# Kernel tuning notes

Measured on AMD Instinct MI355X. Metric: run time of the kernel, lower is better.

The kernel has to match this reference:

```python
import jax, jax.numpy as jnp
import numpy as np

B, L, D = 1, 2048, 1024
H, E = 16, 64        # n_heads, d_head
ROT = E // 2         # rotary half-dim
FF = 4 * D
EPS = 1e-6
NEG = -1e30


def setup_inputs() -> dict:
    key = jax.random.key(0)
    ks = jax.random.split(key, 6)
    x = jax.random.normal(ks[0], (B, L, D), jnp.float32)
    theta = jax.random.uniform(ks[1], (B, H, L, ROT), jnp.float32) * (2.0 * np.pi)
    scale = jax.random.normal(ks[2], (B, D), jnp.float32) * 0.1
    w_in = jax.random.normal(ks[3], (7 * D, D), jnp.float32) * (D ** -0.5)
    w_out = jax.random.normal(ks[4], (D, 5 * D), jnp.float32) * ((5 * D) ** -0.5)
    attn_scale = jnp.full((2, H), 10.0, jnp.float32)
    return {"x": x, "theta": theta, "scale": scale,
            "w_in": w_in, "w_out": w_out, "attn_scale": attn_scale}


def _rope(t, cos, sin):
    # t: [b,h,l,E]; rotary applied to first 2*ROT dims (== E here, so no passthrough)
    t1, t2 = t[..., :ROT], t[..., ROT:2 * ROT]
    return jnp.concatenate([t1 * cos - t2 * sin, t2 * cos + t1 * sin], axis=-1)


def _forward(x, theta, scale, w_in, w_out, attn_scale):
    b, l, d = x.shape
    skip = x
    # AdaRMSNorm (no learned weight): rms-normalize then modulate by (1 + scale)
    xn = x * jax.lax.rsqrt(jnp.mean(x ** 2, axis=-1, keepdims=True) + EPS)
    xn = xn * (1.0 + scale[:, None, :])
    # fused QKV + MLP-up projection (torch Linear: y = x @ W.T)
    proj = jnp.einsum('bld,fd->blf', xn, w_in)       # [b,l,7d]
    qkv, up = proj[..., :3 * d], proj[..., 3 * d:]
    up = jax.nn.gelu(up, approximate=True)           # GELU(tanh)
    # 'b l (t nh e) -> t b nh l e'
    qkv = qkv.reshape(b, l, 3, H, E).transpose(2, 0, 3, 1, 4)
    q, k, v = qkv[0], qkv[1], qkv[2]
    # cosine-sim rescaling: q_h * sqrt(s_h)/||q||, k_h * sqrt(s_h)/||k||
    s = jnp.sqrt(attn_scale[0])[None, :, None, None]
    q = q * (s * jax.lax.rsqrt(jnp.sum(q ** 2, axis=-1, keepdims=True) + EPS))
    k = k * (s * jax.lax.rsqrt(jnp.sum(k ** 2, axis=-1, keepdims=True) + EPS))
    # rotary embedding
    cos, sin = jnp.cos(theta), jnp.sin(theta)
    q, k = _rope(q, cos, sin), _rope(k, cos, sin)
    # causal attention with scale = 1.0 (cosine-sim path)
    scores = jnp.einsum('bhqe,bhke->bhqk', q, k)
    causal = jnp.tril(jnp.ones((l, l), bool))
    scores = jnp.where(causal[None, None], scores, NEG)
    probs = jax.nn.softmax(scores, axis=-1)
    attn = jnp.einsum('bhqk,bhke->bhqe', probs, v)
    attn_out = attn.transpose(0, 2, 1, 3).reshape(b, l, d)  # 'b nh l e -> b l (nh e)'
    h = jnp.concatenate([attn_out, up], axis=-1)            # [b,l,5d]
    return jnp.einsum('blf,df->bld', h, w_out) + skip


def reference(x, theta, scale, w_in, w_out, attn_scale):
    return _forward(x, theta, scale, w_in, w_out, attn_scale)
```

## Files before the change

### kernel.cpp

```cpp
#include <hip/hip_runtime.h>

typedef unsigned short u16;
typedef unsigned int u32;
typedef __attribute__((ext_vector_type(8))) short bf16x8;
typedef __attribute__((ext_vector_type(8))) unsigned short u16x8;
typedef __attribute__((ext_vector_type(4))) float f32x4;
typedef __attribute__((ext_vector_type(16))) float f32x16;

#define L_SEQ 2048
#define DMODEL 1024
#define NHEAD 16
#define EHEAD 64
#define FPROJ 7168
#define FCAT 5120
#define NEGINF -1e30f
#define LOG2E 1.44269504088896f
#define EXP2F(x) __builtin_amdgcn_exp2f(x)

__device__ __forceinline__ u16 f2bf(float f) {
  union { float f; u32 u; } v; v.f = f;
  u32 r = v.u + 0x7FFFu + ((v.u >> 16) & 1u);
  return (u16)(r >> 16);
}
__device__ __forceinline__ float bf2f(u16 h) {
  union { u32 u; float f; } v; v.u = ((u32)h) << 16;
  return v.f;
}
__device__ __forceinline__ float gelu_f(float x) {
  float y = 0.7978845608028654f * (x + 0.044715f * x * x * x);
  float t = __expf(-2.0f * fabsf(y));
  float th = (1.0f - t) / (1.0f + t);
  th = (y < 0.0f) ? -th : th;
  return 0.5f * x * (1.0f + th);
}
__device__ __forceinline__ void gld16(void* lds, const void* g) {
  __builtin_amdgcn_global_load_lds((const __attribute__((address_space(1))) u32*)g,
                                   (__attribute__((address_space(3))) u32*)lds, 16, 0, 0);
}

__global__ __launch_bounds__(256) void cvt2_kernel(const float* __restrict__ a,
                                                   u16* __restrict__ oa, int na4,
                                                   const float* __restrict__ b,
                                                   u16* __restrict__ ob, int nb4) {
  int i = blockIdx.x * 256 + threadIdx.x;
  const float* src;
  u16* dst;
  int j;
  if (i < na4) {
    src = a; dst = oa; j = i;
  } else {
    j = i - na4;
    if (j >= nb4) return;
    src = b; dst = ob;
  }
  float4 v = ((const float4*)src)[j];
  ((u32*)dst)[2 * j] = (u32)f2bf(v.x) | ((u32)f2bf(v.y) << 16);
  ((u32*)dst)[2 * j + 1] = (u32)f2bf(v.z) | ((u32)f2bf(v.w) << 16);
}

__global__ __launch_bounds__(256) void rmsnorm_kernel(const float* __restrict__ x,
                                                      const float* __restrict__ scale,
                                                      u16* __restrict__ xn) {
  int row = blockIdx.x;
  const float4 v = ((const float4*)(x + (size_t)row * DMODEL))[threadIdx.x];
  float ss = v.x * v.x + v.y * v.y + v.z * v.z + v.w * v.w;
#pragma unroll
  for (int m = 1; m < 64; m <<= 1) ss += __shfl_xor(ss, m);
  __shared__ float ws[4];
  if ((threadIdx.x & 63) == 0) ws[threadIdx.x >> 6] = ss;
  __syncthreads();
  float tot = ws[0] + ws[1] + ws[2] + ws[3];
  float r = rsqrtf(tot * (1.0f / DMODEL) + 1e-6f);
  float4 sc = ((const float4*)scale)[threadIdx.x];
  u32 w0 = (u32)f2bf(v.x * r * (1.0f + sc.x)) | ((u32)f2bf(v.y * r * (1.0f + sc.y)) << 16);
  u32 w1 = (u32)f2bf(v.z * r * (1.0f + sc.z)) | ((u32)f2bf(v.w * r * (1.0f + sc.w)) << 16);
  u32* dst = (u32*)(xn + (size_t)row * DMODEL);
  dst[2 * threadIdx.x] = w0;
  dst[2 * threadIdx.x + 1] = w1;
}

__device__ __forceinline__ void stage_half(u16* lds, const u16* g, int K, int tid) {
#pragma unroll
  for (int i = 0; i < 2; ++i) {
    int idx = tid + i * 512;
    int r = idx >> 3;
    int gcb = ((idx & 7) << 4) ^ ((r & 7) << 4);
    gld16((char*)lds + idx * 16, (const char*)g + (size_t)r * K * 2 + gcb);
  }
}

#define GFENCE asm volatile("" ::: "memory")
#define VMW0 asm volatile("s_waitcnt vmcnt(0)" ::: "memory")
#define ST_A(BUF, T, HALF) stage_half(sA + (BUF) * 16384 + (HALF) * 8192, \
    Ab + (size_t)((HALF) * 128) * K + (T) * 64, K, tid)
#define ST_B(BUF, T, HALF) stage_half(sB + (BUF) * 16384 + (HALF) * 8192, \
    Bb + (size_t)((HALF) * 128) * K + (T) * 64, K, tid)

#define PHASE(KH, BUFB, WCODE, STCODE) do { \
    const char* ab_ = (const char*)sA + (BUFB) * 32768 + wm * 16384 + frow * 128 + ((KH) ? co1 : co0); \
    const char* bb_ = (const char*)sB + (BUFB) * 32768 + (wn2 >> 1) * 16384 + ((wn2 & 1) * 64 + frow) * 128 + ((KH) ? co1 : co0); \
    bf16x8 af_[8], bv_[4]; \
    _Pragma("unroll") \
    for (int mr = 0; mr < 8; ++mr) af_[mr] = *(const bf16x8*)(ab_ + mr * 2048); \
    _Pragma("unroll") \
    for (int nr = 0; nr < 4; ++nr) bv_[nr] = *(const bf16x8*)(bb_ + nr * 2048); \
    GFENCE; \
    STCODE; \
    WCODE; \
    __builtin_amdgcn_s_barrier(); \
    __builtin_amdgcn_s_setprio(1); \
    _Pragma("unroll") \
    for (int mr = 0; mr < 8; ++mr) \
      _Pragma("unroll") \
      for (int nr = 0; nr < 4; ++nr) \
        acc[mr][nr] = __builtin_amdgcn_mfma_f32_16x16x32_bf16(af_[mr], bv_[nr], acc[mr][nr], 0, 0, 0); \
    __builtin_amdgcn_s_setprio(0); \
    __builtin_amdgcn_s_barrier(); \
  } while (0)

template <int OUTMODE>
__global__ __launch_bounds__(512, 2) void gemm256(const u16* __restrict__ A,
                                                  const u16* __restrict__ B,
                                                  u16* __restrict__ C0,
                                                  u16* __restrict__ C1,
                                                  int M, int N, int K) {
  __shared__ __align__(16) u16 sA[2 * 16384];
  __shared__ __align__(16) u16 sB[2 * 16384];
  const int tid = threadIdx.x;
  const int lane = tid & 63;
  const int wv = tid >> 6;
  const int wm = wv >> 2;
  const int wn2 = wv & 3;
  const int frow = lane & 15;
  const int kbyte = ((lane >> 4) & 3) << 4;
  const int sw = (frow & 7) << 4;
  const int co0 = kbyte ^ sw;
  const int co1 = (64 | kbyte) ^ sw;

  const int nbx = N >> 8;
  const int nbm = (int)gridDim.x / nbx;
  const int v = (blockIdx.x & 7) * ((int)gridDim.x >> 3) + ((int)blockIdx.x >> 3);
  const int bm = v % nbm, bn = v / nbm;
  const int kper = K / (int)gridDim.y;
  const int kbeg = blockIdx.y * kper;
  const u16* Ab = A + (size_t)(bm * 256) * K + kbeg;
  const u16* Bb = B + (size_t)(bn * 256) * K + kbeg;

  f32x4 acc[8][4] = {};

  const int NT = kper >> 6;
  ST_A(0, 0, 0); ST_A(0, 0, 1); ST_B(0, 0, 0); ST_B(0, 0, 1);
  VMW0;
  __builtin_amdgcn_s_barrier();

  for (int kt = 0; kt < NT; kt += 2) {
    const int t1 = kt + 1;
    const int t2 = (kt + 2 >= NT) ? 0 : kt + 2;
    PHASE(0, 0, , ST_A(1, t1, 0); ST_A(1, t1, 1); ST_B(1, t1, 0); ST_B(1, t1, 1));
    PHASE(1, 0, VMW0, );
    PHASE(0, 1, , ST_A(0, t2, 0); ST_A(0, t2, 1); ST_B(0, t2, 0); ST_B(0, t2, 1));
    PHASE(1, 1, VMW0, );
  }

  if (OUTMODE == 1) {
    const bool up = (bn >= 12);
#pragma unroll
    for (int mr = 0; mr < 8; ++mr) {
#pragma unroll
      for (int nr = 0; nr < 4; ++nr) {
        int grow = bm * 256 + wm * 128 + mr * 16 + ((lane >> 4) * 4);
        int gcol = bn * 256 + wn2 * 64 + nr * 16 + frow;
        if (!up) {
          u16* cp = C0 + (size_t)grow * (3 * DMODEL) + gcol;
#pragma unroll
          for (int r = 0; r < 4; ++r) cp[(size_t)r * (3 * DMODEL)] = f2bf(acc[mr][nr][r]);
        } else {
          u16* cp = C1 + (size_t)grow * FCAT + (gcol - 2048);
#pragma unroll
          for (int r = 0; r < 4; ++r) cp[(size_t)r * FCAT] = f2bf(gelu_f(acc[mr][nr][r]));
        }
      }
    }
  } else {
    u16* Cp = C0 + (size_t)blockIdx.y * M * N;
#pragma unroll
    for (int mr = 0; mr < 8; ++mr) {
#pragma unroll
      for (int nr = 0; nr < 4; ++nr) {
        int grow = bm * 256 + wm * 128 + mr * 16 + ((lane >> 4) * 4);
        int gcol = bn * 256 + wn2 * 64 + nr * 16 + frow;
        u16* cp = Cp + (size_t)grow * N + gcol;
#pragma unroll
        for (int r = 0; r < 4; ++r) cp[(size_t)r * N] = f2bf(acc[mr][nr][r]);
      }
    }
  }
}

__global__ __launch_bounds__(256) void combine8(const u16* __restrict__ part,
                                                const float* __restrict__ x,
                                                float* __restrict__ out) {
  size_t i = (size_t)(blockIdx.x * 256 + threadIdx.x) * 8;
  float4 x0 = *(const float4*)(x + i);
  float4 x1 = *(const float4*)(x + i + 4);
  float s[8] = {x0.x, x0.y, x0.z, x0.w, x1.x, x1.y, x1.z, x1.w};
#pragma unroll
  for (int p = 0; p < 8; ++p) {
    u16x8 v = *(const u16x8*)(part + (size_t)p * (L_SEQ * DMODEL) + i);
#pragma unroll
    for (int j = 0; j < 8; ++j) s[j] += bf2f(v[j]);
  }
  float4 o0 = {s[0], s[1], s[2], s[3]};
  float4 o1 = {s[4], s[5], s[6], s[7]};
  *(float4*)(out + i) = o0;
  *(float4*)(out + i + 4) = o1;
}

__global__ __launch_bounds__(256) void qkv_prep(const u16* __restrict__ proj,
                                                const float* __restrict__ theta,
                                                const float* __restrict__ attn_scale,
                                                u16* __restrict__ qb, u16* __restrict__ kb,
                                                u16* __restrict__ vb) {
  const int l = blockIdx.x * 4 + (threadIdx.x >> 6);
  const int hd = blockIdx.y;
  const int e = threadIdx.x & 63;
  const u16* pr = proj + (size_t)l * (3 * DMODEL) + hd * EHEAD + e;
  float q = bf2f(pr[0]);
  float k = bf2f(pr[DMODEL]);
  float v = bf2f(pr[2 * DMODEL]);
  float sq = q * q, sk = k * k;
#pragma unroll
  for (int m = 1; m < 64; m <<= 1) {
    sq += __shfl_xor(sq, m);
    sk += __shfl_xor(sk, m);
  }
  float s = sqrtf(attn_scale[hd]);
  q *= LOG2E * s * rsqrtf(sq + 1e-6f);
  k *= s * rsqrtf(sk + 1e-6f);
  float ang = theta[((size_t)hd * L_SEQ + l) * 32 + (e & 31)];
  float cs = __cosf(ang), sn = __sinf(ang);
  float qp = __shfl_xor(q, 32), kp = __shfl_xor(k, 32);
  float qr = (e < 32) ? (q * cs - qp * sn) : (q * cs + qp * sn);
  float kr = (e < 32) ? (k * cs - kp * sn) : (k * cs + kp * sn);
  size_t o = ((size_t)hd * L_SEQ + l) * EHEAD + e;
  qb[o] = f2bf(qr);
  kb[o] = f2bf(kr);
  vb[o] = f2bf(v);
}

__global__ __launch_bounds__(128, 4) void attn_kernel(const u16* __restrict__ qb,
                                                      const u16* __restrict__ kb,
                                                      const u16* __restrict__ vb,
                                                      u16* __restrict__ po,
                                                      float* __restrict__ pm,
                                                      float* __restrict__ pl) {
  const int bid = blockIdx.x;
  const int s = 31 - (bid >> 6);
  const int hd = (bid >> 2) & 15;
  const int c = bid & 3;
  const int tid = threadIdx.x;
  const int lane = tid & 63;
  const int w = tid >> 6;
  const int h = lane >> 5;
  const int ql = lane & 31;
  const int qg = s * 64 + w * 32 + ql;
  const int nt = s + 1;
  const int t0 = (c * nt) >> 2;
  const int t1 = ((c + 1) * nt) >> 2;

  __shared__ u16 sK[64 * 64];
  __shared__ u16 sVT[64 * 64];

  const u16* Kh = kb + (size_t)hd * L_SEQ * EHEAD;
  const u16* Vh = vb + (size_t)hd * L_SEQ * EHEAD;
  const u16* Qh = qb + (size_t)hd * L_SEQ * EHEAD;

  bf16x8 qf[4];
#pragma unroll
  for (int es = 0; es < 4; ++es)
    qf[es] = *(const bf16x8*)(Qh + (size_t)qg * EHEAD + es * 16 + h * 8);

  f32x16 oa[2] = {};
  float m = NEGINF, lsum = 0.0f;

  const int vk = (tid & 15) * 4;
  const int ve = (tid >> 4) * 8;

  for (int kt = t0; kt < t1; ++kt) {
    const int k0 = kt * 64;
    __syncthreads();
#pragma unroll
    for (int i = 0; i < 4; ++i) {
      int r = w * 32 + i * 8 + (lane >> 3);
      const u16* src = Kh + (size_t)(k0 + r) * EHEAD + (((lane & 7) ^ (r & 7)) << 3);
      gld16(sK + (w * 32 + i * 8) * 64 + lane * 8, src);
    }
    u16x8 vr[4];
#pragma unroll
    for (int j = 0; j < 4; ++j)
      vr[j] = *(const u16x8*)(Vh + (size_t)(k0 + vk + j) * EHEAD + ve);
#pragma unroll
    for (int e = 0; e < 8; ++e) {
      int row = ve + e;
      int boff = row * 128 + ((((vk >> 3) ^ (row & 7)) << 4) | ((vk & 4) << 1));
      ushort4 pv;
      pv.x = vr[0][e]; pv.y = vr[1][e]; pv.z = vr[2][e]; pv.w = vr[3][e];
      *(ushort4*)((char*)sVT + boff) = pv;
    }
    __syncthreads();

    f32x16 st[2];
#pragma unroll
    for (int t = 0; t < 2; ++t) {
      f32x16 a = {};
      __builtin_amdgcn_s_setprio(1);
#pragma unroll
      for (int es = 0; es < 4; ++es) {
        int row = t * 32 + ql;
        int boff = row * 128 + (((es * 2 + h) ^ (row & 7)) << 4);
        bf16x8 kf = *(const bf16x8*)((const char*)sK + boff);
        a = __builtin_amdgcn_mfma_f32_32x32x16_bf16(kf, qf[es], a, 0, 0, 0);
      }
      __builtin_amdgcn_s_setprio(0);
      st[t] = a;
    }

    float p[2][16];
    float mx = NEGINF;
    const bool edge = (kt == s);
#pragma unroll
    for (int t = 0; t < 2; ++t)
#pragma unroll
      for (int r = 0; r < 16; ++r) {
        float v = st[t][r];
        if (edge) {
          int kg = k0 + t * 32 + (r & 3) + ((r >> 2) << 3) + h * 4;
          v = (kg > qg) ? NEGINF : v;
        }
        p[t][r] = v;
        mx = fmaxf(mx, v);
      }
    mx = fmaxf(mx, __shfl_xor(mx, 32));
    if (!__all(mx - m <= 8.0f)) {
      float mnew = fmaxf(m, mx);
      float alpha = EXP2F(m - mnew);
      lsum *= alpha;
#pragma unroll
      for (int et = 0; et < 2; ++et)
#pragma unroll
        for (int r = 0; r < 16; ++r) oa[et][r] *= alpha;
      m = mnew;
    }
    float ps = 0.0f;
#pragma unroll
    for (int t = 0; t < 2; ++t)
#pragma unroll
      for (int r = 0; r < 16; ++r) {
        float e_ = EXP2F(p[t][r] - m);
        p[t][r] = e_;
        ps += e_;
      }
    ps += __shfl_xor(ps, 32);
    lsum += ps;

    u32 pk_[2][8];
#pragma unroll
    for (int t = 0; t < 2; ++t)
#pragma unroll
      for (int i = 0; i < 8; ++i)
        asm("v_cvt_pk_bf16_f32 %0, %1, %2" : "=v"(pk_[t][i]) : "v"(p[t][2 * i]), "v"(p[t][2 * i + 1]));

#pragma unroll
    for (int ks = 0; ks < 4; ++ks) {
      const int tp = ks >> 1, base = (ks & 1) * 4;
      u32 s0 = h ? pk_[tp][base + 0] : pk_[tp][base + 2];
      u32 s1 = h ? pk_[tp][base + 1] : pk_[tp][base + 3];
      u32 r0 = (u32)__shfl_xor((int)s0, 32);
      u32 r1 = (u32)__shfl_xor((int)s1, 32);
      union { u32 u[4]; bf16x8 v; } pf;
      pf.u[0] = h ? r0 : pk_[tp][base + 0];
      pf.u[1] = h ? r1 : pk_[tp][base + 1];
      pf.u[2] = h ? pk_[tp][base + 2] : r0;
      pf.u[3] = h ? pk_[tp][base + 3] : r1;
      __builtin_amdgcn_s_setprio(1);
#pragma unroll
      for (int et = 0; et < 2; ++et) {
        int row = et * 32 + ql;
        int boff = row * 128 + (((ks * 2 + h) ^ (row & 7)) << 4);
        bf16x8 vf = *(const bf16x8*)((const char*)sVT + boff);
        oa[et] = __builtin_amdgcn_mfma_f32_32x32x16_bf16(vf, pf.v, oa[et], 0, 0, 0);
      }
      __builtin_amdgcn_s_setprio(0);
    }
  }

  const size_t pidx = (size_t)(s * 16 + hd) * 4 + c;
  u16* orow = po + pidx * 4096 + (size_t)(w * 32 + ql) * 64;
#pragma unroll
  for (int et = 0; et < 2; ++et)
#pragma unroll
    for (int g = 0; g < 4; ++g) {
      ushort4 ov;
      ov.x = f2bf(oa[et][4 * g + 0]);
      ov.y = f2bf(oa[et][4 * g + 1]);
      ov.z = f2bf(oa[et][4 * g + 2]);
      ov.w = f2bf(oa[et][4 * g + 3]);
      *(ushort4*)(orow + et * 32 + g * 8 + h * 4) = ov;
    }
  if (h == 0) {
    pm[pidx * 64 + w * 32 + ql] = m;
    pl[pidx * 64 + w * 32 + ql] = lsum;
  }
}

__global__ __launch_bounds__(256) void attn_merge(const u16* __restrict__ po,
                                                  const float* __restrict__ pm,
                                                  const float* __restrict__ pl,
                                                  u16* __restrict__ hb) {
  const int sh = blockIdx.x;
  const int s = sh >> 4, hd = sh & 15;
  const int r = threadIdx.x >> 2;
  const int ec = (threadIdx.x & 3) << 4;
  float mc[4], wgt[4];
  float M = NEGINF;
#pragma unroll
  for (int c = 0; c < 4; ++c) {
    mc[c] = pm[(size_t)(sh * 4 + c) * 64 + r];
    M = fmaxf(M, mc[c]);
  }
  float L = 0.0f;
#pragma unroll
  for (int c = 0; c < 4; ++c) {
    wgt[c] = EXP2F(mc[c] - M);
    L += pl[(size_t)(sh * 4 + c) * 64 + r] * wgt[c];
  }
  float inv = 1.0f / L;
  float o[16] = {};
#pragma unroll
  for (int c = 0; c < 4; ++c) {
    const u16* pp = po + (size_t)(sh * 4 + c) * 4096 + r * 64 + ec;
    u16x8 v0 = *(const u16x8*)pp;
    u16x8 v1 = *(const u16x8*)(pp + 8);
#pragma unroll
    for (int j = 0; j < 8; ++j) {
      o[j] += wgt[c] * bf2f(v0[j]);
      o[8 + j] += wgt[c] * bf2f(v1[j]);
    }
  }
  u16* dst = hb + (size_t)(s * 64 + r) * FCAT + hd * EHEAD + ec;
  u16x8 out0, out1;
#pragma unroll
  for (int j = 0; j < 8; ++j) {
    out0[j] = f2bf(o[j] * inv);
    out1[j] = f2bf(o[8 + j] * inv);
  }
  *(u16x8*)dst = out0;
  *(u16x8*)(dst + 8) = out1;
}

extern "C" void kernel_launch(void* const* d_in, const int* in_sizes, int n_in,
                              void* d_out, int out_size, void* d_ws, size_t ws_size,
                              hipStream_t stream) {
  const float* x = (const float*)d_in[0];
  const float* theta = (const float*)d_in[1];
  const float* scale = (const float*)d_in[2];
  const float* w_in = (const float*)d_in[3];
  const float* w_out = (const float*)d_in[4];
  const float* attn_scale = (const float*)d_in[5];
  float* out = (float*)d_out;

  char* ws = (char*)d_ws;
  u16* w_out_b = (u16*)ws;   ws += (size_t)DMODEL * FCAT * 2;
  u16* hb = (u16*)ws;        ws += (size_t)L_SEQ * FCAT * 2;
  u16* xn = (u16*)ws;        ws += (size_t)L_SEQ * DMODEL * 2;
  u16* w_in_b = (u16*)ws;    ws += (size_t)FPROJ * DMODEL * 2;
  u16* proj = (u16*)ws;      ws += (size_t)L_SEQ * 3 * DMODEL * 2;
  u16* qb = (u16*)ws;        ws += (size_t)NHEAD * L_SEQ * EHEAD * 2;
  u16* kb = (u16*)ws;        ws += (size_t)NHEAD * L_SEQ * EHEAD * 2;
  u16* vb = (u16*)ws;        ws += (size_t)NHEAD * L_SEQ * EHEAD * 2;
  u16* po = xn;
  float* pm = (float*)(po + (size_t)512 * 4 * 4096);
  float* pl = pm + 512 * 4 * 64;
  u16* part = xn;

  const int na4 = FPROJ * DMODEL / 4, nb4 = DMODEL * FCAT / 4;
  cvt2_kernel<<<(na4 + nb4 + 255) / 256, 256, 0, stream>>>(w_in, w_in_b, na4,
                                                           w_out, w_out_b, nb4);
  rmsnorm_kernel<<<L_SEQ, 256, 0, stream>>>(x, scale, xn);
  gemm256<1><<<(L_SEQ / 256) * (FPROJ / 256), 512, 0, stream>>>(xn, w_in_b, proj, hb,
                                                                L_SEQ, FPROJ, DMODEL);
  qkv_prep<<<dim3(L_SEQ / 4, NHEAD), 256, 0, stream>>>(proj, theta, attn_scale, qb, kb, vb);
  attn_kernel<<<2048, 128, 0, stream>>>(qb, kb, vb, po, pm, pl);
  attn_merge<<<512, 256, 0, stream>>>(po, pm, pl, hb);
  gemm256<2><<<dim3((L_SEQ / 256) * (DMODEL / 256), 8), 512, 0, stream>>>(hb, w_out_b, part,
                                                                          nullptr, L_SEQ, DMODEL, FCAT);
  combine8<<<L_SEQ * DMODEL / 8 / 256, 256, 0, stream>>>(part, x, out);
}
```

Measured before the change: 141.2 us.

## Replace 256x256 GEMM tiles with 128x128 tiles and reduce split-K to four

Both GEMMs now use 128x128 output tiles computed by 256 threads with a BK=32 double-buffered LDS pipeline and a simpler per-iteration loop, instead of 256x256 tiles with BK=64 and 512 threads. The projection GEMM goes from 224 blocks to 896, and the output GEMM drops split-K from 8 to 4, so the combine kernel reads fewer partial buffers. The goal is to fill more CUs and cut partial-sum traffic. In exchange, the smaller tiles reuse each loaded operand less and there are more barriers per unit of work.

Measured after the change: 147.7 us. +4.6%, slower.

```diff
diff --git a/kernel.cpp b/kernel.cpp
--- a/kernel.cpp
+++ b/kernel.cpp
@@ -79,97 +79,84 @@
   dst[2 * threadIdx.x + 1] = w1;
 }
 
-__device__ __forceinline__ void stage_half(u16* lds, const u16* g, int K, int tid) {
+__device__ __forceinline__ void stage32(u16* lds, const char* g, int K2, int tid) {
 #pragma unroll
   for (int i = 0; i < 2; ++i) {
-    int idx = tid + i * 512;
-    int r = idx >> 3;
-    int gcb = ((idx & 7) << 4) ^ ((r & 7) << 4);
-    gld16((char*)lds + idx * 16, (const char*)g + (size_t)r * K * 2 + gcb);
+    int s = tid + i * 256;
+    int r = s >> 2, c = s & 3;
+    gld16((char*)lds + s * 16, g + (size_t)r * K2 + ((c ^ (r & 3)) << 4));
   }
 }
 
 #define GFENCE asm volatile("" ::: "memory")
 #define VMW0 asm volatile("s_waitcnt vmcnt(0)" ::: "memory")
-#define ST_A(BUF, T, HALF) stage_half(sA + (BUF) * 16384 + (HALF) * 8192, \
-    Ab + (size_t)((HALF) * 128) * K + (T) * 64, K, tid)
-#define ST_B(BUF, T, HALF) stage_half(sB + (BUF) * 16384 + (HALF) * 8192, \
-    Bb + (size_t)((HALF) * 128) * K + (T) * 64, K, tid)
-
-#define PHASE(KH, BUFB, WCODE, STCODE) do { \
-    const char* ab_ = (const char*)sA + (BUFB) * 32768 + wm * 16384 + frow * 128 + ((KH) ? co1 : co0); \
-    const char* bb_ = (const char*)sB + (BUFB) * 32768 + (wn2 >> 1) * 16384 + ((wn2 & 1) * 64 + frow) * 128 + ((KH) ? co1 : co0); \
-    bf16x8 af_[8], bv_[4]; \
-    _Pragma("unroll") \
-    for (int mr = 0; mr < 8; ++mr) af_[mr] = *(const bf16x8*)(ab_ + mr * 2048); \
-    _Pragma("unroll") \
-    for (int nr = 0; nr < 4; ++nr) bv_[nr] = *(const bf16x8*)(bb_ + nr * 2048); \
-    GFENCE; \
-    STCODE; \
-    WCODE; \
-    __builtin_amdgcn_s_barrier(); \
-    __builtin_amdgcn_s_setprio(1); \
-    _Pragma("unroll") \
-    for (int mr = 0; mr < 8; ++mr) \
-      _Pragma("unroll") \
-      for (int nr = 0; nr < 4; ++nr) \
-        acc[mr][nr] = __builtin_amdgcn_mfma_f32_16x16x32_bf16(af_[mr], bv_[nr], acc[mr][nr], 0, 0, 0); \
-    __builtin_amdgcn_s_setprio(0); \
-    __builtin_amdgcn_s_barrier(); \
-  } while (0)
 
 template <int OUTMODE>
-__global__ __launch_bounds__(512, 2) void gemm256(const u16* __restrict__ A,
+__global__ __launch_bounds__(256, 3) void gemm128(const u16* __restrict__ A,
                                                   const u16* __restrict__ B,
                                                   u16* __restrict__ C0,
                                                   u16* __restrict__ C1,
                                                   int M, int N, int K) {
-  __shared__ __align__(16) u16 sA[2 * 16384];
-  __shared__ __align__(16) u16 sB[2 * 16384];
+  __shared__ __align__(16) u16 sA[2 * 4096];
+  __shared__ __align__(16) u16 sB[2 * 4096];
   const int tid = threadIdx.x;
   const int lane = tid & 63;
   const int wv = tid >> 6;
-  const int wm = wv >> 2;
-  const int wn2 = wv & 3;
+  const int wm = wv >> 1;
+  const int wn2 = wv & 1;
   const int frow = lane & 15;
-  const int kbyte = ((lane >> 4) & 3) << 4;
-  const int sw = (frow & 7) << 4;
-  const int co0 = kbyte ^ sw;
-  const int co1 = (64 | kbyte) ^ sw;
-
-  const int nbx = N >> 8;
-  const int nbm = (int)gridDim.x / nbx;
+  const int co = (((lane >> 4) ^ (frow & 3)) << 4);
+
+  const int nbm = M >> 7;
   const int v = (blockIdx.x & 7) * ((int)gridDim.x >> 3) + ((int)blockIdx.x >> 3);
   const int bm = v % nbm, bn = v / nbm;
   const int kper = K / (int)gridDim.y;
   const int kbeg = blockIdx.y * kper;
-  const u16* Ab = A + (size_t)(bm * 256) * K + kbeg;
-  const u16* Bb = B + (size_t)(bn * 256) * K + kbeg;
-
-  f32x4 acc[8][4] = {};
-
-  const int NT = kper >> 6;
-  ST_A(0, 0, 0); ST_A(0, 0, 1); ST_B(0, 0, 0); ST_B(0, 0, 1);
+  const int K2 = K * 2;
+  const u16* Ab = A + (size_t)(bm * 128) * K + kbeg;
+  const u16* Bb = B + (size_t)(bn * 128) * K + kbeg;
+
+  f32x4 acc[4][4] = {};
+
+  const int NT = kper >> 5;
+  stage32(sA, (const char*)Ab, K2, tid);
+  stage32(sB, (const char*)Bb, K2, tid);
   VMW0;
   __builtin_amdgcn_s_barrier();
 
-  for (int kt = 0; kt < NT; kt += 2) {
-    const int t1 = kt + 1;
-    const int t2 = (kt + 2 >= NT) ? 0 : kt + 2;
-    PHASE(0, 0, , ST_A(1, t1, 0); ST_A(1, t1, 1); ST_B(1, t1, 0); ST_B(1, t1, 1));
-    PHASE(1, 0, VMW0, );
-    PHASE(0, 1, , ST_A(0, t2, 0); ST_A(0, t2, 1); ST_B(0, t2, 0); ST_B(0, t2, 1));
-    PHASE(1, 1, VMW0, );
-  }
-
+  for (int kt = 0; kt < NT; ++kt) {
+    const int buf = kt & 1;
+    const int tn = (kt + 1 < NT) ? kt + 1 : 0;
+    stage32(sA + (buf ^ 1) * 4096, (const char*)(Ab + tn * 32), K2, tid);
+    stage32(sB + (buf ^ 1) * 4096, (const char*)(Bb + tn * 32), K2, tid);
+    const char* ap = (const char*)sA + buf * 8192 + (wm * 64 + frow) * 64 + co;
+    const char* bp = (const char*)sB + buf * 8192 + (wn2 * 64 + frow) * 64 + co;
+    bf16x8 af[4], bv[4];
+#pragma unroll
+    for (int mr = 0; mr < 4; ++mr) af[mr] = *(const bf16x8*)(ap + mr * 1024);
+#pragma unroll
+    for (int nr = 0; nr < 4; ++nr) bv[nr] = *(const bf16x8*)(bp + nr * 1024);
+    GFENCE;
+    __builtin_amdgcn_s_setprio(1);
+#pragma unroll
+    for (int mr = 0; mr < 4; ++mr)
+#pragma unroll
+      for (int nr = 0; nr < 4; ++nr)
+        acc[mr][nr] = __builtin_amdgcn_mfma_f32_16x16x32_bf16(af[mr], bv[nr], acc[mr][nr], 0, 0, 0);
+    __builtin_amdgcn_s_setprio(0);
+    VMW0;
+    __builtin_amdgcn_s_barrier();
+  }
+
+  const int r0 = (lane >> 4) * 4;
   if (OUTMODE == 1) {
-    const bool up = (bn >= 12);
-#pragma unroll
-    for (int mr = 0; mr < 8; ++mr) {
+    const bool up = (bn >= 24);
+#pragma unroll
+    for (int mr = 0; mr < 4; ++mr) {
 #pragma unroll
       for (int nr = 0; nr < 4; ++nr) {
-        int grow = bm * 256 + wm * 128 + mr * 16 + ((lane >> 4) * 4);
-        int gcol = bn * 256 + wn2 * 64 + nr * 16 + frow;
+        int grow = bm * 128 + wm * 64 + mr * 16 + r0;
+        int gcol = bn * 128 + wn2 * 64 + nr * 16 + frow;
         if (!up) {
           u16* cp = C0 + (size_t)grow * (3 * DMODEL) + gcol;
 #pragma unroll
@@ -184,11 +171,11 @@
   } else {
     u16* Cp = C0 + (size_t)blockIdx.y * M * N;
 #pragma unroll
-    for (int mr = 0; mr < 8; ++mr) {
+    for (int mr = 0; mr < 4; ++mr) {
 #pragma unroll
       for (int nr = 0; nr < 4; ++nr) {
-        int grow = bm * 256 + wm * 128 + mr * 16 + ((lane >> 4) * 4);
-        int gcol = bn * 256 + wn2 * 64 + nr * 16 + frow;
+        int grow = bm * 128 + wm * 64 + mr * 16 + r0;
+        int gcol = bn * 128 + wn2 * 64 + nr * 16 + frow;
         u16* cp = Cp + (size_t)grow * N + gcol;
 #pragma unroll
         for (int r = 0; r < 4; ++r) cp[(size_t)r * N] = f2bf(acc[mr][nr][r]);
@@ -197,7 +184,7 @@
   }
 }
 
-__global__ __launch_bounds__(256) void combine8(const u16* __restrict__ part,
+__global__ __launch_bounds__(256) void combine4(const u16* __restrict__ part,
                                                 const float* __restrict__ x,
                                                 float* __restrict__ out) {
   size_t i = (size_t)(blockIdx.x * 256 + threadIdx.x) * 8;
@@ -205,7 +192,7 @@
   float4 x1 = *(const float4*)(x + i + 4);
   float s[8] = {x0.x, x0.y, x0.z, x0.w, x1.x, x1.y, x1.z, x1.w};
 #pragma unroll
-  for (int p = 0; p < 8; ++p) {
+  for (int p = 0; p < 4; ++p) {
     u16x8 v = *(const u16x8*)(part + (size_t)p * (L_SEQ * DMODEL) + i);
 #pragma unroll
     for (int j = 0; j < 8; ++j) s[j] += bf2f(v[j]);
@@ -487,12 +474,12 @@
   cvt2_kernel<<<(na4 + nb4 + 255) / 256, 256, 0, stream>>>(w_in, w_in_b, na4,
                                                            w_out, w_out_b, nb4);
   rmsnorm_kernel<<<L_SEQ, 256, 0, stream>>>(x, scale, xn);
-  gemm256<1><<<(L_SEQ / 256) * (FPROJ / 256), 512, 0, stream>>>(xn, w_in_b, proj, hb,
-                                                                L_SEQ, FPROJ, DMODEL);
+  gemm128<1><<<dim3((L_SEQ / 128) * (FPROJ / 128), 1), 256, 0, stream>>>(
+      xn, w_in_b, proj, hb, L_SEQ, FPROJ, DMODEL);
   qkv_prep<<<dim3(L_SEQ / 4, NHEAD), 256, 0, stream>>>(proj, theta, attn_scale, qb, kb, vb);
   attn_kernel<<<2048, 128, 0, stream>>>(qb, kb, vb, po, pm, pl);
   attn_merge<<<512, 256, 0, stream>>>(po, pm, pl, hb);
-  gemm256<2><<<dim3((L_SEQ / 256) * (DMODEL / 256), 8), 512, 0, stream>>>(hb, w_out_b, part,
-                                                                          nullptr, L_SEQ, DMODEL, FCAT);
-  combine8<<<L_SEQ * DMODEL / 8 / 256, 256, 0, stream>>>(part, x, out);
-}
+  gemm128<2><<<dim3((L_SEQ / 128) * (DMODEL / 128), 4), 256, 0, stream>>>(
+      hb, w_out_b, part, nullptr, L_SEQ, DMODEL, FCAT);
+  combine4<<<L_SEQ * DMODEL / 8 / 256, 256, 0, stream>>>(part, x, out);
+}
```
